# Kernel tuning notes

Measured on AMD Instinct MI355X. Metric: run time of the kernel, lower is better.

## Reference

```python
import jax, jax.numpy as jnp
import numpy as np

S, B, D, H, DH = 2048, 2, 1024, 16, 64


def setup_inputs() -> dict:
    key = jax.random.key(0)
    ks = jax.random.split(key, 7)
    sc = 0.02
    return {
        "x": jax.random.normal(ks[0], (S, B, D), jnp.float32),
        "pos_emb": jax.random.normal(ks[1], (S, D), jnp.float32),
        "pos_bias_u": jax.random.normal(ks[2], (H, DH), jnp.float32) * sc,
        "pos_bias_v": jax.random.normal(ks[3], (H, DH), jnp.float32) * sc,
        "W_qkv": jax.random.normal(ks[4], (D, 3 * H * DH), jnp.float32) * sc,
        "W_relemb": jax.random.normal(ks[5], (D, H * DH), jnp.float32) * sc,
        "W_o": jax.random.normal(ks[6], (H * DH, D), jnp.float32) * sc,
        "ln_gamma": jnp.ones((D,), jnp.float32),
        "ln_beta": jnp.zeros((D,), jnp.float32),
    }


def _rel_shift(x):
    # x: [i, j, b, n]; Transformer-XL relative shift
    i, j, b, n = x.shape
    zero_pad = jnp.zeros((i, 1, b, n), x.dtype)
    xp = jnp.concatenate([zero_pad, x], axis=1)      # [i, j+1, b, n]
    xp = xp.reshape(j + 1, i, b, n)
    return xp[1:].reshape(i, j, b, n)


def reference(x, pos_emb, pos_bias_u, pos_bias_v, W_qkv, W_relemb, W_o, ln_gamma, ln_beta):
    seq_len, batch, d_model = x.shape
    num_head, d_head = pos_bias_u.shape
    scale = jnp.asarray(1.0 / d_head ** 0.5, x.dtype)

    qkv = x @ W_qkv                                   # [S,B,3*H*DH]
    q, k, v = jnp.split(qkv, 3, axis=-1)
    q = q.reshape(seq_len, batch, num_head, d_head)
    k = k.reshape(seq_len, batch, num_head, d_head)
    v = v.reshape(seq_len, batch, num_head, d_head)
    r = (pos_emb @ W_relemb).reshape(seq_len, num_head, d_head)

    AC = jnp.einsum('ibnd,jbnd->ijbn', q + pos_bias_u, k)
    BD = _rel_shift(jnp.einsum('ibnd,jnd->ijbn', q + pos_bias_v, r))
    attn_score = (AC + BD) * scale                    # [S,S,B,H]
    attn_prob = jax.nn.softmax(attn_score, axis=1)

    attn_vec = jnp.einsum('ijbn,jbnd->ibnd', attn_prob, v)
    attn_vec = attn_vec.reshape(seq_len, batch, num_head * d_head)
    attn_out = attn_vec @ W_o

    y = x + attn_out
    mu = jnp.mean(y, axis=-1, keepdims=True)
    var = jnp.mean(jnp.square(y - mu), axis=-1, keepdims=True)
    y_norm = (y - mu) * jax.lax.rsqrt(var + 1e-5)
    return y_norm * ln_gamma + ln_beta
```

## Files before the change

kernel.cpp:

```cpp
#include <hip/hip_runtime.h>
#include <stdint.h>

#define S_LEN 2048
#define BATCH 2
#define DMODEL 1024
#define NHEAD 16
#define DHEAD 64
#define HS ((size_t)S_LEN * DHEAD)

typedef float floatx4 __attribute__((ext_vector_type(4)));
typedef __bf16 bf16x8 __attribute__((ext_vector_type(8)));

typedef __attribute__((address_space(1))) const uint32_t gas_u32;
typedef __attribute__((address_space(3))) uint32_t las_u32;
__device__ __forceinline__ void gld_lds16(const uint16_t* g, uint16_t* l) {
  __builtin_amdgcn_global_load_lds((gas_u32*)g, (las_u32*)l, 16, 0, 0);
}

__device__ __forceinline__ float bf2f(uint16_t u) {
  union { uint32_t i; float f; } x; x.i = ((uint32_t)u) << 16; return x.f;
}
__device__ __forceinline__ uint16_t f2bf(float f) {
  union { float f; uint32_t i; } x; x.f = f;
  uint32_t r = x.i + 0x7fffu + ((x.i >> 16) & 1u);
  return (uint16_t)(r >> 16);
}
__device__ __forceinline__ uint16_t f2bf_hw(float f) {
  __bf16 h = (__bf16)f;
  union { __bf16 h; uint16_t u; } c; c.h = h; return c.u;
}
__device__ __forceinline__ uint4 ld8(const void* p, size_t idx, int isf32) {
  if (isf32) {
    const float* f = (const float*)p + idx;
    float4 a = *(const float4*)f;
    float4 b = *(const float4*)(f + 4);
    uint4 r; uint16_t* rp = (uint16_t*)&r;
    rp[0] = f2bf(a.x); rp[1] = f2bf(a.y); rp[2] = f2bf(a.z); rp[3] = f2bf(a.w);
    rp[4] = f2bf(b.x); rp[5] = f2bf(b.y); rp[6] = f2bf(b.z); rp[7] = f2bf(b.w);
    return r;
  }
  return *(const uint4*)((const uint16_t*)p + idx);
}
__device__ __forceinline__ float ld1(const void* p, size_t idx, int isf32) {
  return isf32 ? ((const float*)p)[idx] : bf2f(((const uint16_t*)p)[idx]);
}
__device__ __forceinline__ uint4 addb8(uint4 a, uint4 b) {
  uint4 r;
  const uint16_t* pa = (const uint16_t*)&a;
  const uint16_t* pb = (const uint16_t*)&b;
  uint16_t* pr = (uint16_t*)&r;
#pragma unroll
  for (int e = 0; e < 8; e++) pr[e] = f2bf(bf2f(pa[e]) + bf2f(pb[e]));
  return r;
}

__global__ __launch_bounds__(256) void detect_dtype(const void* __restrict__ x,
                                                    int* __restrict__ flag) {
  __shared__ int cnt;
  if (threadIdx.x == 0) cnt = 0;
  __syncthreads();
  const uint16_t w = ((const uint16_t*)x)[threadIdx.x];
  const float v = bf2f(w);
  const float av = fabsf(v);
  if (!(av <= 256.f)) atomicAdd(&cnt, 1);
  __syncthreads();
  if (threadIdx.x == 0) *flag = (cnt >= 8) ? 1 : 0;
}

__global__ __launch_bounds__(256) void cvt_x(const void* __restrict__ x,
                                             uint16_t* __restrict__ xb,
                                             const int* __restrict__ pflag) {
  const int isf32 = *pflag;
  const size_t gid = (size_t)blockIdx.x * 256 + threadIdx.x;
  const int d0 = (int)(gid & (DMODEL / 8 - 1)) * 8;
  const size_t sb = gid >> 7;
  const size_t s = sb >> 1, b = sb & 1;
  uint4 v = ld8(x, sb * DMODEL + d0, isf32);
  *(uint4*)&xb[(b * S_LEN + s) * DMODEL + d0] = v;
}

__global__ __launch_bounds__(256) void cvt_mat(const void* __restrict__ src,
                                               uint16_t* __restrict__ dst,
                                               const int* __restrict__ pflag) {
  const int isf32 = *pflag;
  const size_t gid = ((size_t)blockIdx.x * 256 + threadIdx.x) * 8;
  *(uint4*)&dst[gid] = ld8(src, gid, isf32);
}

__global__ __launch_bounds__(256) void cvt_matT(const void* __restrict__ src,
                                                uint16_t* __restrict__ dst,
                                                int R, int C,
                                                const int* __restrict__ pflag) {
  __shared__ uint16_t lT[64 * 72];
  const int isf32 = *pflag;
  const int tid = threadIdx.x;
  const int c0 = blockIdx.x * 64;
  const int r0 = blockIdx.y * 64;
  {
    const int rr = tid >> 2, cc = (tid & 3) * 16;
    *(uint4*)&lT[rr * 72 + cc]     = ld8(src, (size_t)(r0 + rr) * C + c0 + cc, isf32);
    *(uint4*)&lT[rr * 72 + cc + 8] = ld8(src, (size_t)(r0 + rr) * C + c0 + cc + 8, isf32);
  }
  __syncthreads();
  const int oc = tid >> 2, rc = (tid & 3) * 16;
  uint16_t tmp[16];
#pragma unroll
  for (int e = 0; e < 16; e++) tmp[e] = lT[(rc + e) * 72 + oc];
  uint16_t* dp = dst + (size_t)(c0 + oc) * R + r0 + rc;
  *(uint4*)dp = *(const uint4*)&tmp[0];
  *(uint4*)(dp + 8) = *(const uint4*)&tmp[8];
}

__global__ __launch_bounds__(256) void qkv_gemm(
    const uint16_t* __restrict__ xb, const uint16_t* __restrict__ peb,
    const uint16_t* __restrict__ wqT, const uint16_t* __restrict__ wrT,
    uint16_t* __restrict__ qb, uint16_t* __restrict__ kb,
    uint16_t* __restrict__ vb, uint16_t* __restrict__ rb, int z0) {
  __shared__ uint16_t lA[128 * 32];
  __shared__ uint16_t lB[128 * 40];
  const int tid = threadIdx.x;
  const int lane = tid & 63;
  const int wave = tid >> 6;
  const int wm = wave >> 1, wn = wave & 1;
  const int strip = blockIdx.x;
  const int zg0 = z0 + 2 * blockIdx.z;
  const int b = zg0 >> 4, h0 = zg0 & 15;

  const uint16_t* Ab;
  const uint16_t* BT;
  int col0;
  if (strip < 3) {
    Ab = xb + (size_t)b * S_LEN * DMODEL;
    BT = wqT; col0 = strip * DMODEL + h0 * 64;
  } else {
    Ab = peb;
    BT = wrT; col0 = h0 * 64;
  }
  Ab += (size_t)blockIdx.y * 128 * DMODEL;

  floatx4 acc[4][4];
  floatx4 zero4 = {0.f, 0.f, 0.f, 0.f};
#pragma unroll
  for (int i = 0; i < 4; i++)
#pragma unroll
    for (int j = 0; j < 4; j++) acc[i][j] = zero4;

  const int arow = tid >> 2;
  const int kcol = (tid & 3) * 8;
  const int brow = tid >> 1;
  const int bkc = (tid & 1) * 16;

  for (int k0 = 0; k0 < DMODEL; k0 += 32) {
    gld_lds16(Ab + (size_t)arow * DMODEL + k0 + kcol, &lA[wave * 512]);
    gld_lds16(Ab + (size_t)(64 + arow) * DMODEL + k0 + kcol, &lA[2048 + wave * 512]);
    const uint16_t* bp = BT + (size_t)(col0 + brow) * DMODEL + k0 + bkc;
    *(uint4*)&lB[brow * 40 + bkc]     = *(const uint4*)bp;
    *(uint4*)&lB[brow * 40 + bkc + 8] = *(const uint4*)(bp + 8);
    __syncthreads();
    bf16x8 af[4], bfr[4];
#pragma unroll
    for (int mi = 0; mi < 4; mi++)
      af[mi] = *(const bf16x8*)&lA[(wm * 64 + mi * 16 + (lane & 15)) * 32 + (lane >> 4) * 8];
#pragma unroll
    for (int ni = 0; ni < 4; ni++)
      bfr[ni] = *(const bf16x8*)&lB[(wn * 64 + ni * 16 + (lane & 15)) * 40 + (lane >> 4) * 8];
#pragma unroll
    for (int mi = 0; mi < 4; mi++)
#pragma unroll
      for (int ni = 0; ni < 4; ni++)
        acc[mi][ni] = __builtin_amdgcn_mfma_f32_16x16x32_bf16(af[mi], bfr[ni], acc[mi][ni], 0, 0, 0);
    __syncthreads();
  }

  uint16_t* ob = (strip == 0) ? qb : (strip == 1) ? kb : (strip == 2) ? vb : rb;
  const int r0 = blockIdx.y * 128 + wm * 64;
  const int zlb = 2 * blockIdx.z;
#pragma unroll
  for (int mi = 0; mi < 4; mi++)
#pragma unroll
    for (int ni = 0; ni < 4; ni++)
#pragma unroll
      for (int v = 0; v < 4; v++) {
        const int sg = r0 + mi * 16 + (lane >> 4) * 4 + v;
        const int c  = wn * 64 + ni * 16 + (lane & 15);
        const int zl = zlb + (c >> 6);
        const int d  = c & 63;
        ob[(size_t)zl * HS + (size_t)sg * 64 + d] = f2bf_hw(acc[mi][ni][v]);
      }
}

__global__ __launch_bounds__(256) void transpose_v(const uint16_t* __restrict__ vb,
                                                   uint16_t* __restrict__ vt) {
  __shared__ uint16_t lT[64 * 72];
  const int tid = threadIdx.x;
  const int zl = blockIdx.y;
  const int j0 = blockIdx.x * 64;
  const uint16_t* src = vb + (size_t)zl * HS + (size_t)j0 * 64;
  {
    const int j = tid >> 2, dc = (tid & 3) * 16;
    *(uint4*)&lT[j * 72 + dc] = *(const uint4*)(src + (size_t)j * 64 + dc);
    *(uint4*)&lT[j * 72 + dc + 8] = *(const uint4*)(src + (size_t)j * 64 + dc + 8);
  }
  __syncthreads();
  const int d = tid >> 2, jc = (tid & 3) * 16;
  uint16_t tmp[16];
#pragma unroll
  for (int e = 0; e < 16; e++) tmp[e] = lT[(jc + e) * 72 + d];
  uint16_t* dst = vt + (size_t)zl * HS + (size_t)d * S_LEN + j0 + jc;
  *(uint4*)dst = *(const uint4*)&tmp[0];
  *(uint4*)(dst + 8) = *(const uint4*)&tmp[8];
}

#define FBP 72
#define VTP 136
#define PBP 132
#define SC2 0.180336880f

#define FA_ISSUE(bxn) do {                                                  \
    const uint16_t* spk_ = kz + (size_t)((bxn) * 128 + sj) * 64 + skc;      \
    kr0 = *(const uint4*)spk_;                                              \
    kr1 = *(const uint4*)(spk_ + 8);                                        \
    const uint16_t* spv_ = vz + (size_t)sd * S_LEN + (bxn) * 128 + sjc;     \
    vr0 = *(const uint4*)spv_;                                              \
    vr1 = *(const uint4*)(spv_ + 8);                                        \
    const int Dq_ = ((bxn) - by) * 128 + sslot - 127;                       \
    int rrow_ = (Dq_ <= 0) ? (Dq_ + S_LEN - 1) : (Dq_ - 2 < 0 ? 0 : Dq_ - 2); \
    if (rrow_ > S_LEN - 1) rrow_ = S_LEN - 1;                               \
    const uint16_t* spr_ = rz + (size_t)rrow_ * 64 + shalf;                 \
    br0 = *(const uint4*)spr_;                                              \
    br1 = *(const uint4*)(spr_ + 8);                                        \
    br2 = *(const uint4*)(spr_ + 16);                                       \
    br3 = *(const uint4*)(spr_ + 24);                                       \
  } while (0)

#define FA_COMMIT() do {                                                    \
    *(uint4*)&lK[sj * FBP + skc]     = kr0;                                 \
    *(uint4*)&lK[sj * FBP + skc + 8] = kr1;                                 \
    *(uint4*)&lV[sd * VTP + sjc]     = vr0;                                 \
    *(uint4*)&lV[sd * VTP + sjc + 8] = vr1;                                 \
    uint16_t* dp_ = &lR[sslot * FBP + shalf];                               \
    *(uint4*)(dp_)      = br0;                                              \
    *(uint4*)(dp_ + 8)  = br1;                                              \
    *(uint4*)(dp_ + 16) = br2;                                              \
    *(uint4*)(dp_ + 24) = br3;                                              \
  } while (0)

__global__ __launch_bounds__(512, 2) void flash_attn(
    const uint16_t* __restrict__ qb, const uint16_t* __restrict__ kb,
    const uint16_t* __restrict__ vt, const uint16_t* __restrict__ rb,
    const void* __restrict__ bu, const void* __restrict__ bv,
    uint16_t* __restrict__ avec, int z0, int zc,
    const int* __restrict__ pflag) {
  __shared__ uint16_t lK[128 * FBP];
  __shared__ uint16_t lV[64 * VTP];
  __shared__ uint16_t lR[256 * FBP];
  __shared__ uint16_t lP[8 * 16 * PBP];
  const int isf32 = *pflag;
  const int tid = threadIdx.x;
  const int lane = tid & 63;
  const int w = tid >> 6;
  const int l15 = lane & 15;
  const int l4 = lane >> 4;
  int by, zl;
  {
    const int bid = blockIdx.x;
    if ((zc & 7) == 0) {
      const int xcd = bid & 7;
      const int t = bid >> 3;
      by = t & 15;
      zl = xcd + 8 * (t >> 4);
    } else {
      by = bid & 15;
      zl = bid >> 4;
    }
  }
  const int zg = z0 + zl;
  const int b = zg >> 4, h = zg & 15;
  const int i0 = by * 128;

  const uint16_t* qz = qb + (size_t)zl * HS;
  const uint16_t* kz = kb + (size_t)zl * HS;
  const uint16_t* vz = vt + (size_t)zl * HS;
  const uint16_t* rz = rb + (size_t)zl * HS;
  uint16_t* pbw = lP + w * 16 * PBP;
  const int cmin = 112 - 16 * w;
  const int r_loc = l4 * 4;

  const int sj = tid >> 2, skc = (tid & 3) * 16;
  const int sd = tid >> 3, sjc = (tid & 7) * 16;
  const int sslot = tid >> 1, shalf = (tid & 1) * 32;

  uint4 kr0, kr1, vr0, vr1, br0, br1, br2, br3;

  uint4 af1[2], af2[2], af2s[2];
  {
    const int qrow = i0 + w * 16 + l15;
    const int qrow1 = min(qrow + 1, S_LEN - 1);
#pragma unroll
    for (int ks = 0; ks < 2; ks++) {
      const int kc = ks * 32 + l4 * 8;
      uint4 bub = ld8(bu, (size_t)h * 64 + kc, isf32);
      uint4 bvb = ld8(bv, (size_t)h * 64 + kc, isf32);
      uint4 qv  = *(const uint4*)(qz + (size_t)qrow * 64 + kc);
      uint4 qv1 = *(const uint4*)(qz + (size_t)qrow1 * 64 + kc);
      af1[ks]  = addb8(qv, bub);
      af2[ks]  = addb8(qv, bvb);
      af2s[ks] = addb8(qv1, bvb);
    }
  }

  floatx4 acc_o[4];
  floatx4 zero4 = {0.f, 0.f, 0.f, 0.f};
#pragma unroll
  for (int i = 0; i < 4; i++) acc_o[i] = zero4;
  float m[4] = {-1e30f, -1e30f, -1e30f, -1e30f};
  float l[4] = {0.f, 0.f, 0.f, 0.f};

  FA_ISSUE(0);
  FA_COMMIT();
  __syncthreads();

  for (int bx = 0; bx < 16; ++bx) {
    const int del = bx - by;
    if (bx < 15) FA_ISSUE(bx + 1);

    floatx4 accp[9];
#pragma unroll
    for (int f = 0; f < 9; f++) accp[f] = zero4;
#pragma unroll
    for (int ks = 0; ks < 2; ks++) {
      const bf16x8 a1 = *(const bf16x8*)&af2[ks];
      const bf16x8 a2 = *(const bf16x8*)&af2s[ks];
#pragma unroll
      for (int f = 0; f < 9; f++) {
        const int cb = cmin + 16 * f;
        const bf16x8 brg = *(const bf16x8*)&lR[(cb + l15) * FBP + ks * 32 + l4 * 8];
        const bf16x8 a = (cb >= 128 - 128 * del) ? a2 : a1;
        accp[f] = __builtin_amdgcn_mfma_f32_16x16x32_bf16(a, brg, accp[f], 0, 0, 0);
      }
    }
    floatx4 acc_s[8];
#pragma unroll
    for (int f = 0; f < 8; f++) acc_s[f] = zero4;
#pragma unroll
    for (int ks = 0; ks < 2; ks++) {
      const bf16x8 a = *(const bf16x8*)&af1[ks];
#pragma unroll
      for (int f = 0; f < 8; f++) {
        const bf16x8 bk = *(const bf16x8*)&lK[(f * 16 + l15) * FBP + ks * 32 + l4 * 8];
        acc_s[f] = __builtin_amdgcn_mfma_f32_16x16x32_bf16(a, bk, acc_s[f], 0, 0, 0);
      }
    }

    float rmax[4] = {-1e30f, -1e30f, -1e30f, -1e30f};
#pragma unroll
    for (int v = 0; v < 4; v++) {
      const int r = r_loc + v;
      const int srcl = l4 * 16 + ((l15 + 15 - r) & 15);
      float sh[9];
#pragma unroll
      for (int f = 0; f < 9; f++) sh[f] = __shfl(accp[f][v], srcl);
      const int Dbase = del * 128 + l15 - w * 16 - r;
#pragma unroll
      for (int f = 0; f < 8; f++) {
        float bd = (l15 <= r) ? sh[f] : sh[f + 1];
        if (Dbase + 16 * f == 1) bd = 0.f;
        const float sv = (acc_s[f][v] + bd) * SC2;
        acc_s[f][v] = sv;
        rmax[v] = fmaxf(rmax[v], sv);
      }
    }
#pragma unroll
    for (int v = 0; v < 4; v++) {
#pragma unroll
      for (int o = 1; o < 16; o <<= 1) rmax[v] = fmaxf(rmax[v], __shfl_xor(rmax[v], o));
      const float mn = fmaxf(m[v], rmax[v]);
      const float al = __builtin_amdgcn_exp2f(m[v] - mn);
      m[v] = mn;
      l[v] *= al;
#pragma unroll
      for (int nd = 0; nd < 4; nd++) acc_o[nd][v] *= al;
    }
    float rsum[4] = {0.f, 0.f, 0.f, 0.f};
#pragma unroll
    for (int f = 0; f < 8; f++)
#pragma unroll
      for (int v = 0; v < 4; v++) {
        const float p = __builtin_amdgcn_exp2f(acc_s[f][v] - m[v]);
        acc_s[f][v] = p;
        rsum[v] += p;
      }
#pragma unroll
    for (int v = 0; v < 4; v++) {
#pragma unroll
      for (int o = 1; o < 16; o <<= 1) rsum[v] += __shfl_xor(rsum[v], o);
      l[v] += rsum[v];
    }
#pragma unroll
    for (int f = 0; f < 8; f++)
#pragma unroll
      for (int v = 0; v < 4; v++)
        pbw[(r_loc + v) * PBP + f * 16 + l15] = f2bf_hw(acc_s[f][v]);

#pragma unroll
    for (int ks = 0; ks < 4; ks++) {
      const bf16x8 ap = *(const bf16x8*)&pbw[l15 * PBP + ks * 32 + l4 * 8];
#pragma unroll
      for (int nd = 0; nd < 4; nd++) {
        const bf16x8 bvv = *(const bf16x8*)&lV[(nd * 16 + l15) * VTP + ks * 32 + l4 * 8];
        acc_o[nd] = __builtin_amdgcn_mfma_f32_16x16x32_bf16(ap, bvv, acc_o[nd], 0, 0, 0);
      }
    }

    __syncthreads();
    if (bx < 15) {
      FA_COMMIT();
      __syncthreads();
    }
  }

#pragma unroll
  for (int v = 0; v < 4; v++) {
    const float inv = 1.f / l[v];
    const int i = i0 + w * 16 + r_loc + v;
#pragma unroll
    for (int nd = 0; nd < 4; nd++) {
      const int d = nd * 16 + l15;
      avec[((size_t)i * BATCH + b) * DMODEL + h * 64 + d] = f2bf_hw(acc_o[nd][v] * inv);
    }
  }
}

__global__ __launch_bounds__(256) void out_gemm(
    const uint16_t* __restrict__ avec, const uint16_t* __restrict__ woT,
    const void* __restrict__ x, uint16_t* __restrict__ ybuf,
    const int* __restrict__ pflag) {
  __shared__ uint16_t lA[128 * 32];
  __shared__ uint16_t lB[128 * 40];
  const int isf32 = *pflag;
  const int tid = threadIdx.x;
  const int lane = tid & 63;
  const int wave = tid >> 6;
  const int wm = wave >> 1, wn = wave & 1;
  const uint16_t* Ab = avec + (size_t)blockIdx.y * 128 * DMODEL;
  const int col0 = blockIdx.x * 128;

  floatx4 acc[4][4];
  floatx4 zero4 = {0.f, 0.f, 0.f, 0.f};
#pragma unroll
  for (int i = 0; i < 4; i++)
#pragma unroll
    for (int j = 0; j < 4; j++) acc[i][j] = zero4;

  const int arow = tid >> 2;
  const int kcol = (tid & 3) * 8;
  const int brow = tid >> 1;
  const int bkc = (tid & 1) * 16;

  for (int k0 = 0; k0 < DMODEL; k0 += 32) {
    gld_lds16(Ab + (size_t)arow * DMODEL + k0 + kcol, &lA[wave * 512]);
    gld_lds16(Ab + (size_t)(64 + arow) * DMODEL + k0 + kcol, &lA[2048 + wave * 512]);
    const uint16_t* bp = woT + (size_t)(col0 + brow) * DMODEL + k0 + bkc;
    *(uint4*)&lB[brow * 40 + bkc]     = *(const uint4*)bp;
    *(uint4*)&lB[brow * 40 + bkc + 8] = *(const uint4*)(bp + 8);
    __syncthreads();
    bf16x8 af[4], bfr[4];
#pragma unroll
    for (int mi = 0; mi < 4; mi++)
      af[mi] = *(const bf16x8*)&lA[(wm * 64 + mi * 16 + (lane & 15)) * 32 + (lane >> 4) * 8];
#pragma unroll
    for (int ni = 0; ni < 4; ni++)
      bfr[ni] = *(const bf16x8*)&lB[(wn * 64 + ni * 16 + (lane & 15)) * 40 + (lane >> 4) * 8];
#pragma unroll
    for (int mi = 0; mi < 4; mi++)
#pragma unroll
      for (int ni = 0; ni < 4; ni++)
        acc[mi][ni] = __builtin_amdgcn_mfma_f32_16x16x32_bf16(af[mi], bfr[ni], acc[mi][ni], 0, 0, 0);
    __syncthreads();
  }

  const int r0 = blockIdx.y * 128 + wm * 64;
#pragma unroll
  for (int mi = 0; mi < 4; mi++)
#pragma unroll
    for (int ni = 0; ni < 4; ni++)
#pragma unroll
      for (int v = 0; v < 4; v++) {
        const int rg = r0 + mi * 16 + (lane >> 4) * 4 + v;
        const int cg = col0 + wn * 64 + ni * 16 + (lane & 15);
        const size_t o = (size_t)rg * DMODEL + cg;
        ybuf[o] = f2bf_hw(acc[mi][ni][v] + ld1(x, o, isf32));
      }
}

__global__ __launch_bounds__(256) void ln_f32(
    const uint16_t* __restrict__ y, const void* __restrict__ gamma,
    const void* __restrict__ beta, float* __restrict__ out,
    const int* __restrict__ pflag) {
  const int isf32 = *pflag;
  const int row = blockIdx.x;
  const int tid = threadIdx.x;
  const int lane = tid & 63, wave = tid >> 6;
  const uint16_t* yr = y + (size_t)row * DMODEL;
  uint2 u = *(const uint2*)(yr + tid * 4);
  const uint16_t* up = (const uint16_t*)&u;
  float f[4];
  float s = 0.f, q = 0.f;
#pragma unroll
  for (int j = 0; j < 4; j++) { f[j] = bf2f(up[j]); s += f[j]; q += f[j] * f[j]; }
#pragma unroll
  for (int o = 32; o; o >>= 1) { s += __shfl_xor(s, o); q += __shfl_xor(q, o); }
  __shared__ float rs[4], rq[4];
  if (lane == 0) { rs[wave] = s; rq[wave] = q; }
  __syncthreads();
  s = rs[0] + rs[1] + rs[2] + rs[3];
  q = rq[0] + rq[1] + rq[2] + rq[3];
  const float mu = s * (1.f / DMODEL);
  const float var = fmaxf(q * (1.f / DMODEL) - mu * mu, 0.f);
  const float inv = rsqrtf(var + 1e-5f);
  float4 o4;
  float* op = (float*)&o4;
#pragma unroll
  for (int j = 0; j < 4; j++) {
    const int c = tid * 4 + j;
    float r = (f[j] - mu) * inv * ld1(gamma, c, isf32) + ld1(beta, c, isf32);
    if (!(r == r)) r = 1e4f;
    op[j] = r;
  }
  *(float4*)(out + (size_t)row * DMODEL + tid * 4) = o4;
}

__global__ __launch_bounds__(256) void sentinel_fill(float* __restrict__ out) {
  const size_t i = (size_t)blockIdx.x * 1024 + threadIdx.x * 4;
  out[i] = 1e6f; out[i + 1] = 1e6f; out[i + 2] = 1e6f; out[i + 3] = 1e6f;
}

extern "C" void kernel_launch(void* const* d_in, const int* in_sizes, int n_in,
                              void* d_out, int out_size, void* d_ws, size_t ws_size,
                              hipStream_t stream) {
  const void* x    = d_in[0];
  const void* pe   = d_in[1];
  const void* bu   = d_in[2];
  const void* bv   = d_in[3];
  const void* Wqkv = d_in[4];
  const void* Wrel = d_in[5];
  const void* Wo   = d_in[6];
  const void* gam  = d_in[7];
  const void* bet  = d_in[8];
  float* out = (float*)d_out;

  const size_t per_z = 5 * HS * 2;
  const size_t conv_bytes = (size_t)(8 + 4 + 6 + 2 + 2) * 1024 * 1024;
  int ZC = 0;
  for (int c = 32; c >= 2; c >>= 1)
    if (256 + (size_t)c * per_z + conv_bytes <= ws_size) { ZC = c; break; }

  const dim3 blk(256);
  if (ZC == 0) {
    sentinel_fill<<<dim3(4096), blk, 0, stream>>>(out);
    return;
  }

  int* flag = (int*)d_ws;
  uint16_t* qb  = (uint16_t*)((char*)d_ws + 256);
  uint16_t* kb  = qb + (size_t)ZC * HS;
  uint16_t* vb  = kb + (size_t)ZC * HS;
  uint16_t* rb  = vb + (size_t)ZC * HS;
  uint16_t* vtb = rb + (size_t)ZC * HS;
  uint16_t* xbuf = vtb + (size_t)ZC * HS;
  uint16_t* peb  = xbuf + (size_t)BATCH * S_LEN * DMODEL;
  uint16_t* wqT  = peb + (size_t)S_LEN * DMODEL;
  uint16_t* wrT  = wqT + (size_t)DMODEL * 3 * DMODEL;
  uint16_t* woT  = wrT + (size_t)DMODEL * DMODEL;
  uint16_t* ybuf = xbuf;
  uint16_t* avec = (uint16_t*)d_out;

  detect_dtype<<<dim3(1), blk, 0, stream>>>(x, flag);
  cvt_x<<<dim3(2048), blk, 0, stream>>>(x, xbuf, flag);
  cvt_mat<<<dim3(1024), blk, 0, stream>>>(pe, peb, flag);
  cvt_matT<<<dim3(48, 16), blk, 0, stream>>>(Wqkv, wqT, DMODEL, 3 * DMODEL, flag);
  cvt_matT<<<dim3(16, 16), blk, 0, stream>>>(Wrel, wrT, DMODEL, DMODEL, flag);
  cvt_matT<<<dim3(16, 16), blk, 0, stream>>>(Wo,   woT, DMODEL, DMODEL, flag);

  for (int z0 = 0; z0 < 32; z0 += ZC) {
    qkv_gemm<<<dim3(4, 16, ZC / 2), blk, 0, stream>>>(xbuf, peb, wqT, wrT,
                                                      qb, kb, vb, rb, z0);
    transpose_v<<<dim3(32, ZC), blk, 0, stream>>>(vb, vtb);
    flash_attn<<<dim3(16 * ZC), dim3(512), 0, stream>>>(qb, kb, vtb, rb, bu, bv,
                                                        avec, z0, ZC, flag);
  }

  out_gemm<<<dim3(8, 32, 1), blk, 0, stream>>>(avec, woT, x, ybuf, flag);
  ln_f32<<<dim3(4096), blk, 0, stream>>>(ybuf, gam, bet, out, flag);
}
```

Measured before the change: 390.9 us.

## Load GEMM B tiles via direct-to-LDS, remap blocks per XCD, dedup rel-emb projection

```diff
diff --git a/kernel.cpp b/kernel.cpp
--- a/kernel.cpp
+++ b/kernel.cpp
@@ -115,16 +115,23 @@
     const uint16_t* __restrict__ xb, const uint16_t* __restrict__ peb,
     const uint16_t* __restrict__ wqT, const uint16_t* __restrict__ wrT,
     uint16_t* __restrict__ qb, uint16_t* __restrict__ kb,
-    uint16_t* __restrict__ vb, uint16_t* __restrict__ rb, int z0) {
+    uint16_t* __restrict__ vb, uint16_t* __restrict__ rb, int z0, int dedup) {
   __shared__ uint16_t lA[128 * 32];
-  __shared__ uint16_t lB[128 * 40];
+  __shared__ uint16_t lB[128 * 32];
   const int tid = threadIdx.x;
   const int lane = tid & 63;
   const int wave = tid >> 6;
   const int wm = wave >> 1, wn = wave & 1;
-  const int strip = blockIdx.x;
-  const int zg0 = z0 + 2 * blockIdx.z;
+  const int bid = blockIdx.x;
+  const int xcd = bid & 7;
+  const int rem = bid >> 3;
+  const int strip = rem & 3;
+  const int gy = xcd + 8 * (rem >> 2);
+  const int by = gy & 15;
+  const int t  = gy >> 4;
+  const int zg0 = z0 + 2 * t;
   const int b = zg0 >> 4, h0 = zg0 & 15;
+  if (strip == 3 && dedup && (zg0 & 16)) return;
 
   const uint16_t* Ab;
   const uint16_t* BT;
@@ -136,7 +143,7 @@
     Ab = peb;
     BT = wrT; col0 = h0 * 64;
   }
-  Ab += (size_t)blockIdx.y * 128 * DMODEL;
+  Ab += (size_t)by * 128 * DMODEL;
 
   floatx4 acc[4][4];
   floatx4 zero4 = {0.f, 0.f, 0.f, 0.f};
@@ -147,23 +154,22 @@
 
   const int arow = tid >> 2;
   const int kcol = (tid & 3) * 8;
-  const int brow = tid >> 1;
-  const int bkc = (tid & 1) * 16;
+  const int l15 = lane & 15;
+  const int l4 = lane >> 4;
 
   for (int k0 = 0; k0 < DMODEL; k0 += 32) {
     gld_lds16(Ab + (size_t)arow * DMODEL + k0 + kcol, &lA[wave * 512]);
     gld_lds16(Ab + (size_t)(64 + arow) * DMODEL + k0 + kcol, &lA[2048 + wave * 512]);
-    const uint16_t* bp = BT + (size_t)(col0 + brow) * DMODEL + k0 + bkc;
-    *(uint4*)&lB[brow * 40 + bkc]     = *(const uint4*)bp;
-    *(uint4*)&lB[brow * 40 + bkc + 8] = *(const uint4*)(bp + 8);
+    gld_lds16(BT + (size_t)(col0 + arow) * DMODEL + k0 + kcol, &lB[wave * 512]);
+    gld_lds16(BT + (size_t)(col0 + 64 + arow) * DMODEL + k0 + kcol, &lB[2048 + wave * 512]);
     __syncthreads();
     bf16x8 af[4], bfr[4];
 #pragma unroll
     for (int mi = 0; mi < 4; mi++)
-      af[mi] = *(const bf16x8*)&lA[(wm * 64 + mi * 16 + (lane & 15)) * 32 + (lane >> 4) * 8];
+      af[mi] = *(const bf16x8*)&lA[(wm * 64 + mi * 16 + l15) * 32 + l4 * 8];
 #pragma unroll
     for (int ni = 0; ni < 4; ni++)
-      bfr[ni] = *(const bf16x8*)&lB[(wn * 64 + ni * 16 + (lane & 15)) * 40 + (lane >> 4) * 8];
+      bfr[ni] = *(const bf16x8*)&lB[(wn * 64 + ni * 16 + l15) * 32 + l4 * 8];
 #pragma unroll
     for (int mi = 0; mi < 4; mi++)
 #pragma unroll
@@ -173,8 +179,8 @@
   }
 
   uint16_t* ob = (strip == 0) ? qb : (strip == 1) ? kb : (strip == 2) ? vb : rb;
-  const int r0 = blockIdx.y * 128 + wm * 64;
-  const int zlb = 2 * blockIdx.z;
+  const int r0 = by * 128 + wm * 64;
+  const int zlb = 2 * t;
 #pragma unroll
   for (int mi = 0; mi < 4; mi++)
 #pragma unroll
@@ -213,7 +219,7 @@
 
 #define FBP 72
 #define VTP 136
-#define PBP 132
+#define PBP 136
 #define SC2 0.180336880f
 
 #define FA_ISSUE(bxn) do {                                                  \
@@ -281,7 +287,7 @@
   const uint16_t* qz = qb + (size_t)zl * HS;
   const uint16_t* kz = kb + (size_t)zl * HS;
   const uint16_t* vz = vt + (size_t)zl * HS;
-  const uint16_t* rz = rb + (size_t)zl * HS;
+  const uint16_t* rz = rb + (size_t)(zc >= 16 ? (zg & 15) : zl) * HS;
   uint16_t* pbw = lP + w * 16 * PBP;
   const int cmin = 112 - 16 * w;
   const int r_loc = l4 * 4;
@@ -436,7 +442,7 @@
     const void* __restrict__ x, uint16_t* __restrict__ ybuf,
     const int* __restrict__ pflag) {
   __shared__ uint16_t lA[128 * 32];
-  __shared__ uint16_t lB[128 * 40];
+  __shared__ uint16_t lB[128 * 32];
   const int isf32 = *pflag;
   const int tid = threadIdx.x;
   const int lane = tid & 63;
@@ -454,23 +460,22 @@
 
   const int arow = tid >> 2;
   const int kcol = (tid & 3) * 8;
-  const int brow = tid >> 1;
-  const int bkc = (tid & 1) * 16;
+  const int l15 = lane & 15;
+  const int l4 = lane >> 4;
 
   for (int k0 = 0; k0 < DMODEL; k0 += 32) {
     gld_lds16(Ab + (size_t)arow * DMODEL + k0 + kcol, &lA[wave * 512]);
     gld_lds16(Ab + (size_t)(64 + arow) * DMODEL + k0 + kcol, &lA[2048 + wave * 512]);
-    const uint16_t* bp = woT + (size_t)(col0 + brow) * DMODEL + k0 + bkc;
-    *(uint4*)&lB[brow * 40 + bkc]     = *(const uint4*)bp;
-    *(uint4*)&lB[brow * 40 + bkc + 8] = *(const uint4*)(bp + 8);
+    gld_lds16(woT + (size_t)(col0 + arow) * DMODEL + k0 + kcol, &lB[wave * 512]);
+    gld_lds16(woT + (size_t)(col0 + 64 + arow) * DMODEL + k0 + kcol, &lB[2048 + wave * 512]);
     __syncthreads();
     bf16x8 af[4], bfr[4];
 #pragma unroll
     for (int mi = 0; mi < 4; mi++)
-      af[mi] = *(const bf16x8*)&lA[(wm * 64 + mi * 16 + (lane & 15)) * 32 + (lane >> 4) * 8];
+      af[mi] = *(const bf16x8*)&lA[(wm * 64 + mi * 16 + l15) * 32 + l4 * 8];
 #pragma unroll
     for (int ni = 0; ni < 4; ni++)
-      bfr[ni] = *(const bf16x8*)&lB[(wn * 64 + ni * 16 + (lane & 15)) * 40 + (lane >> 4) * 8];
+      bfr[ni] = *(const bf16x8*)&lB[(wn * 64 + ni * 16 + l15) * 32 + l4 * 8];
 #pragma unroll
     for (int mi = 0; mi < 4; mi++)
 #pragma unroll
@@ -560,6 +565,7 @@
     sentinel_fill<<<dim3(4096), blk, 0, stream>>>(out);
     return;
   }
+  const int dedup = (ZC >= 16) ? 1 : 0;
 
   int* flag = (int*)d_ws;
   uint16_t* qb  = (uint16_t*)((char*)d_ws + 256);
@@ -583,8 +589,8 @@
   cvt_matT<<<dim3(16, 16), blk, 0, stream>>>(Wo,   woT, DMODEL, DMODEL, flag);
 
   for (int z0 = 0; z0 < 32; z0 += ZC) {
-    qkv_gemm<<<dim3(4, 16, ZC / 2), blk, 0, stream>>>(xbuf, peb, wqT, wrT,
-                                                      qb, kb, vb, rb, z0);
+    qkv_gemm<<<dim3(4 * 16 * (ZC / 2)), blk, 0, stream>>>(xbuf, peb, wqT, wrT,
+                                                          qb, kb, vb, rb, z0, dedup);
     transpose_v<<<dim3(32, ZC), blk, 0, stream>>>(vb, vtb);
     flash_attn<<<dim3(16 * ZC), dim3(512), 0, stream>>>(qb, kb, vtb, rb, bu, bv,
                                                         avec, z0, ZC, flag);
```

Measured after the change: 361.4 us. -7.5%, faster.
